# Optimization experiments

Measured on AMD Instinct MI355X. Metric: run time of the kernel, lower is better.

## Reference

```python
import jax, jax.numpy as jnp
import numpy as np
import math

B, T, E, K, V = 64, 512, 512, 512, 512


def setup_inputs() -> dict:
    key = jax.random.key(0)
    ks = jax.random.split(key, 7)
    s = 1.0 / math.sqrt(E)
    return {
        "x": jax.random.normal(ks[0], (B, T, E), dtype=jnp.float32),
        "Wq": jax.random.normal(ks[1], (E, K), dtype=jnp.float32) * s,
        "bq": jnp.zeros((K,), dtype=jnp.float32),
        "Wk": jax.random.normal(ks[2], (E, K), dtype=jnp.float32) * s,
        "bk": jnp.zeros((K,), dtype=jnp.float32),
        "Wv": jax.random.normal(ks[3], (E, V), dtype=jnp.float32) * s,
        "bv": jnp.zeros((V,), dtype=jnp.float32),
    }


def reference(x, Wq, bq, Wk, bk, Wv, bv):
    # Linear projections (N, T, E) -> (N, T, K/V)
    q = x @ Wq + bq
    k = x @ Wk + bk
    v = x @ Wv + bv
    # weight_pos_graph(query, keys) interpreted as Q K^T: (N, T, T)
    scores = jnp.einsum("btd,bsd->bts", q, k)
    # mask[j, i] = 1 if i > j  -> strict upper triangle masked to -inf (causal)
    mask = jnp.triu(jnp.ones((T, T), dtype=bool), k=1)
    scores = jnp.where(mask, -jnp.inf, scores)
    # NOTE: original softmaxes over dim=1 (the query/row axis), not dim=-1
    attn = jax.nn.softmax(scores / math.sqrt(K), axis=1)
    # bmm(attn, values): (N, T, T) @ (N, T, V) -> (N, T, V)
    return jnp.einsum("bts,bsv->btv", attn, v)
```

## Files before the change

### kernel.cpp

```cpp
#include <hip/hip_runtime.h>
#include <hip/hip_bf16.h>
#include <math.h>

#define B_DIM 64
#define T_DIM 512
#define E_DIM 512

typedef __bf16 bf16_t;
typedef bf16_t bf16x8 __attribute__((ext_vector_type(8)));
typedef float  f32x4  __attribute__((ext_vector_type(4)));

typedef unsigned char __attribute__((address_space(1))) uc_g;
typedef unsigned char __attribute__((address_space(3))) uc_l;

__device__ __forceinline__ void gl_lds16(const void* g, void* l) {
  __builtin_amdgcn_global_load_lds((const uc_g*)g, (uc_l*)l, 16, 0, 0);
}

__global__ __launch_bounds__(256) void cvtx_kernel(const float* __restrict__ x,
                                                   bf16_t* __restrict__ xb) {
  const size_t t = (size_t)blockIdx.x * 256 + threadIdx.x;
  const float4 a = ((const float4*)x)[t * 2];
  const float4 b = ((const float4*)x)[t * 2 + 1];
  bf16x8 o;
  o[0] = (bf16_t)a.x; o[1] = (bf16_t)a.y; o[2] = (bf16_t)a.z; o[3] = (bf16_t)a.w;
  o[4] = (bf16_t)b.x; o[5] = (bf16_t)b.y; o[6] = (bf16_t)b.z; o[7] = (bf16_t)b.w;
  *(bf16x8*)(xb + t * 8) = o;
}

__global__ __launch_bounds__(256) void wtr_kernel(const float* __restrict__ W0,
                                                  const float* __restrict__ W1,
                                                  const float* __restrict__ W2,
                                                  bf16_t* __restrict__ WTall) {
  const int z = blockIdx.z;
  const float* W = z == 0 ? W0 : (z == 1 ? W1 : W2);
  bf16_t* O = WTall + (size_t)z * 512 * E_DIM;
  __shared__ float tile[32][33];
  const int tx = threadIdx.x, ty = threadIdx.y;
  const int r0 = blockIdx.y * 32, c0 = blockIdx.x * 32;
#pragma unroll
  for (int i = 0; i < 4; ++i)
    tile[ty + i * 8][tx] = W[(size_t)(r0 + ty + i * 8) * E_DIM + c0 + tx];
  __syncthreads();
#pragma unroll
  for (int i = 0; i < 4; ++i)
    O[(size_t)(c0 + ty + i * 8) * E_DIM + r0 + tx] = (bf16_t)tile[tx][ty + i * 8];
}

__global__ __launch_bounds__(256) void bcat_kernel(const float* __restrict__ b0,
                                                   const float* __restrict__ b1,
                                                   const float* __restrict__ b2,
                                                   float* __restrict__ bb) {
  const int i = blockIdx.x * 256 + threadIdx.x;
  bb[i] = i < 512 ? b0[i] : (i < 1024 ? b1[i - 512] : b2[i - 1024]);
}

__global__ __launch_bounds__(256) void zero_kernel(float4* __restrict__ p) {
  p[blockIdx.x * 256 + threadIdx.x] = make_float4(0.f, 0.f, 0.f, 0.f);
}

__global__ __launch_bounds__(512) void vtr_kernel(const bf16_t* __restrict__ Vb,
                                                  const float* __restrict__ Dsum,
                                                  bf16_t* __restrict__ VT, int ldv) {
  const int b = blockIdx.z;
  __shared__ bf16_t tile[64][65];
  const int tx = threadIdx.x, ty = threadIdx.y;
  const bf16_t* src = Vb + (size_t)b * T_DIM * ldv;
  const float* Ds = Dsum + (size_t)b * T_DIM;
  bf16_t* dst = VT + (size_t)b * T_DIM * T_DIM;
  const int r0 = blockIdx.y * 64, c0 = blockIdx.x * 64;
#pragma unroll
  for (int i = 0; i < 8; ++i) {
    const int s = r0 + ty + i * 8;
    const float inv = 1.0f / Ds[s];
    tile[ty + i * 8][tx] = (bf16_t)((float)src[(size_t)s * ldv + c0 + tx] * inv);
  }
  __syncthreads();
#pragma unroll
  for (int i = 0; i < 8; ++i)
    dst[(size_t)(c0 + ty + i * 8) * T_DIM + r0 + tx] = tile[tx][ty + i * 8];
}

template <int EPI>
__global__ __launch_bounds__(512)
void gemm_p(const bf16_t* __restrict__ A, const bf16_t* __restrict__ Bt,
            void* __restrict__ Cv, const float* __restrict__ bias,
            float* __restrict__ Dsum,
            int lda, int ldb, int ldc, long sA, long sB, long sC, float scale) {
  __shared__ bf16_t lds[3][12288];
  const int tid = threadIdx.x;

  int bm, bn, bz, NT;
  if (EPI == 0) {
    const int lin = blockIdx.x;
    const int nl = (lin & 7) * 192 + (lin >> 3);
    bm = nl / 6; bn = nl - bm * 6;
    bz = 0; NT = 16;
  } else {
    bm = blockIdx.x; bn = blockIdx.y; bz = blockIdx.z;
    if (EPI == 1 && 2 * bn > bm) return;
    NT = (EPI == 2) ? (bm + 1) * 4 : 16;
  }

  const bf16_t* Ab = A + bz * sA + (long)bm * 128 * lda;
  const bf16_t* Bb = Bt + bz * sB + (long)bn * 256 * ldb;

  const int strow = tid >> 2, stg = tid & 3;
  const int sgg = stg ^ ((strow >> 1) & 3);
  const bf16_t* gA  = Ab + (long)strow * lda + sgg * 8;
  const bf16_t* gB0 = Bb + (long)strow * ldb + sgg * 8;
  const bf16_t* gB1 = gB0 + (long)128 * ldb;

#define STAGE(kt, buf) { gl_lds16(gA  + (long)(kt) * 32, &lds[buf][tid * 8]);        \
                         gl_lds16(gB0 + (long)(kt) * 32, &lds[buf][4096 + tid * 8]); \
                         gl_lds16(gB1 + (long)(kt) * 32, &lds[buf][8192 + tid * 8]); }

  const int l15 = tid & 15, lk = (tid >> 4) & 3;
  const int w = tid >> 6, wr = w >> 2, wc = w & 3;
  int aoff[4], boff[4];
#pragma unroll
  for (int m = 0; m < 4; ++m) {
    const int row = wr * 64 + m * 16 + l15;
    aoff[m] = row * 32 + (lk ^ ((row >> 1) & 3)) * 8;
  }
#pragma unroll
  for (int n = 0; n < 4; ++n) {
    const int row = wc * 64 + n * 16 + l15;
    boff[n] = 4096 + row * 32 + (lk ^ ((row >> 1) & 3)) * 8;
  }

  f32x4 acc[4][4] = {};

  STAGE(0, 0); STAGE(1, 1);
  asm volatile("s_waitcnt vmcnt(3)" ::: "memory");
  asm volatile("s_barrier" ::: "memory");

  int cb = 0;
  for (int kt = 0; kt < NT; ++kt) {
    bf16x8 af[4], bfr[4];
#pragma unroll
    for (int m = 0; m < 4; ++m) af[m] = *(const bf16x8*)&lds[cb][aoff[m]];
#pragma unroll
    for (int n = 0; n < 4; ++n) bfr[n] = *(const bf16x8*)&lds[cb][boff[n]];
    const int sb = (cb == 0) ? 2 : cb - 1;
    if (kt + 2 < NT) {
      STAGE(kt + 2, sb);
      asm volatile("s_waitcnt vmcnt(3)" ::: "memory");
    } else if (kt + 2 == NT) {
      asm volatile("s_waitcnt vmcnt(0)" ::: "memory");
    }
    asm volatile("s_barrier" ::: "memory");
    __builtin_amdgcn_s_setprio(1);
#pragma unroll
    for (int m = 0; m < 4; ++m)
#pragma unroll
      for (int n = 0; n < 4; ++n)
        acc[m][n] = __builtin_amdgcn_mfma_f32_16x16x32_bf16(af[m], bfr[n], acc[m][n], 0, 0, 0);
    __builtin_amdgcn_s_setprio(0);
    asm volatile("s_barrier" ::: "memory");
    cb = (cb == 2) ? 0 : cb + 1;
  }
#undef STAGE

  if constexpr (EPI == 0) {
    bf16_t* C = (bf16_t*)Cv;
#pragma unroll
    for (int m = 0; m < 4; ++m) {
      const long row0 = (long)bm * 128 + wr * 64 + m * 16 + lk * 4;
#pragma unroll
      for (int n = 0; n < 4; ++n) {
        const int col = bn * 256 + wc * 64 + n * 16 + l15;
        const float bv = bias[col];
#pragma unroll
        for (int r = 0; r < 4; ++r)
          C[(row0 + r) * (long)ldc + col] = (bf16_t)(acc[m][n][r] + bv);
      }
    }
  } else if constexpr (EPI == 1) {
    bf16_t* C = (bf16_t*)Cv + bz * sC;
    float ts[4] = {0.f, 0.f, 0.f, 0.f};
#pragma unroll
    for (int m = 0; m < 4; ++m) {
      const long row0 = (long)bm * 128 + wr * 64 + m * 16 + lk * 4;
#pragma unroll
      for (int n = 0; n < 4; ++n) {
        const int lcol = wc * 64 + n * 16 + l15;
        const int col = bn * 256 + lcol;
#pragma unroll
        for (int r = 0; r < 4; ++r) {
          const long row = row0 + r;
          float e = 0.f;
          if (col <= row) e = __expf(acc[m][n][r] * scale);
          const bf16_t eb = (bf16_t)e;
          C[row * (long)ldc + col] = eb;
          ts[n] += (float)eb;
        }
      }
    }
#pragma unroll
    for (int n = 0; n < 4; ++n) {
      ts[n] += __shfl_xor(ts[n], 16);
      ts[n] += __shfl_xor(ts[n], 32);
    }
    float* colsum = (float*)&lds[0][0];
    if (tid < 256) colsum[tid] = 0.f;
    __syncthreads();
    if (lk == 0) {
#pragma unroll
      for (int n = 0; n < 4; ++n)
        atomicAdd(&colsum[wc * 64 + n * 16 + l15], ts[n]);
    }
    __syncthreads();
    if (tid < 256)
      atomicAdd(&Dsum[(long)bz * T_DIM + bn * 256 + tid], colsum[tid]);
  } else {
    float* C = (float*)Cv + bz * sC;
#pragma unroll
    for (int m = 0; m < 4; ++m) {
      const long row0 = (long)bm * 128 + wr * 64 + m * 16 + lk * 4;
#pragma unroll
      for (int n = 0; n < 4; ++n) {
        const int col = bn * 256 + wc * 64 + n * 16 + l15;
#pragma unroll
        for (int r = 0; r < 4; ++r)
          C[(row0 + r) * (long)ldc + col] = acc[m][n][r];
      }
    }
  }
}

extern "C" void kernel_launch(void* const* d_in, const int* in_sizes, int n_in,
                              void* d_out, int out_size, void* d_ws, size_t ws_size,
                              hipStream_t stream) {
  const float* x  = (const float*)d_in[0];
  const float* Wq = (const float*)d_in[1];
  const float* bq = (const float*)d_in[2];
  const float* Wk = (const float*)d_in[3];
  const float* bk = (const float*)d_in[4];
  const float* Wv = (const float*)d_in[5];
  const float* bv = (const float*)d_in[6];
  float* out = (float*)d_out;

  char* ws = (char*)d_ws;
  const size_t SZ = (size_t)B_DIM * T_DIM * E_DIM * 2;
  bf16_t* xb    = (bf16_t*)(ws);
  bf16_t* P     = (bf16_t*)(ws);
  bf16_t* qkv   = (bf16_t*)(ws + SZ);
  bf16_t* vT    = (bf16_t*)(ws + SZ + 3 * SZ);
  bf16_t* WTall = (bf16_t*)(ws + 5 * SZ);
  float*  bcat  = (float*)(ws + 5 * SZ + 1572864);
  float*  Dsum  = (float*)(ws + 5 * SZ + 1572864 + 8192);

  const long sQKV = (long)T_DIM * 1536;
  const long bstr = (long)T_DIM * T_DIM;
  const float scale = 1.0f / sqrtf((float)E_DIM);

  cvtx_kernel<<<dim3(8192), dim3(256), 0, stream>>>(x, xb);
  wtr_kernel<<<dim3(16, 16, 3), dim3(32, 8), 0, stream>>>(Wq, Wk, Wv, WTall);
  bcat_kernel<<<dim3(6), dim3(256), 0, stream>>>(bq, bk, bv, bcat);
  gemm_p<0><<<dim3(1536), dim3(512), 0, stream>>>(
      xb, WTall, qkv, bcat, nullptr, 512, 512, 1536, 0, 0, 0, 0.f);
  zero_kernel<<<dim3(32), dim3(256), 0, stream>>>((float4*)Dsum);
  gemm_p<1><<<dim3(4, 2, B_DIM), dim3(512), 0, stream>>>(
      qkv, qkv + 512, P, nullptr, Dsum, 1536, 1536, T_DIM, sQKV, sQKV, bstr, scale);
  vtr_kernel<<<dim3(8, 8, B_DIM), dim3(64, 8), 0, stream>>>(qkv + 1024, Dsum, vT, 1536);
  gemm_p<2><<<dim3(4, 2, B_DIM), dim3(512), 0, stream>>>(
      P, vT, out, nullptr, nullptr, 512, 512, T_DIM, bstr, bstr, bstr, 1.f);
}
```

Before: 276.0 us.

## Merge prep kernels into one launch and use 256x256 tiled QKV GEMM

Four small preprocessing kernels (x conversion, weight transpose, bias concat, Dsum zeroing) are fused into one prep kernel dispatched by block index, removing launch overhead. The QKV projection moves from the generic 128x256 tile GEMM to a dedicated 256x256 tile kernel with a 64-wide K step, double-buffered 128KB LDS and interleaved half-tile loads and MFMA phases. This raises per-block data reuse and halves the block count, at the cost of one block per CU and more barriers per step.

```diff
diff --git a/kernel.cpp b/kernel.cpp
--- a/kernel.cpp
+++ b/kernel.cpp
@@ -17,46 +17,48 @@
   __builtin_amdgcn_global_load_lds((const uc_g*)g, (uc_l*)l, 16, 0, 0);
 }
 
-__global__ __launch_bounds__(256) void cvtx_kernel(const float* __restrict__ x,
-                                                   bf16_t* __restrict__ xb) {
-  const size_t t = (size_t)blockIdx.x * 256 + threadIdx.x;
-  const float4 a = ((const float4*)x)[t * 2];
-  const float4 b = ((const float4*)x)[t * 2 + 1];
-  bf16x8 o;
-  o[0] = (bf16_t)a.x; o[1] = (bf16_t)a.y; o[2] = (bf16_t)a.z; o[3] = (bf16_t)a.w;
-  o[4] = (bf16_t)b.x; o[5] = (bf16_t)b.y; o[6] = (bf16_t)b.z; o[7] = (bf16_t)b.w;
-  *(bf16x8*)(xb + t * 8) = o;
-}
-
-__global__ __launch_bounds__(256) void wtr_kernel(const float* __restrict__ W0,
-                                                  const float* __restrict__ W1,
-                                                  const float* __restrict__ W2,
-                                                  bf16_t* __restrict__ WTall) {
-  const int z = blockIdx.z;
-  const float* W = z == 0 ? W0 : (z == 1 ? W1 : W2);
-  bf16_t* O = WTall + (size_t)z * 512 * E_DIM;
+__global__ __launch_bounds__(256)
+void prep_kernel(const float* __restrict__ x,
+                 const float* __restrict__ Wq, const float* __restrict__ Wk,
+                 const float* __restrict__ Wv,
+                 const float* __restrict__ bq, const float* __restrict__ bk,
+                 const float* __restrict__ bv,
+                 bf16_t* __restrict__ xb, bf16_t* __restrict__ WTall,
+                 float* __restrict__ bcat, float* __restrict__ Dsum) {
   __shared__ float tile[32][33];
-  const int tx = threadIdx.x, ty = threadIdx.y;
-  const int r0 = blockIdx.y * 32, c0 = blockIdx.x * 32;
-#pragma unroll
-  for (int i = 0; i < 4; ++i)
-    tile[ty + i * 8][tx] = W[(size_t)(r0 + ty + i * 8) * E_DIM + c0 + tx];
-  __syncthreads();
-#pragma unroll
-  for (int i = 0; i < 4; ++i)
-    O[(size_t)(c0 + ty + i * 8) * E_DIM + r0 + tx] = (bf16_t)tile[tx][ty + i * 8];
-}
-
-__global__ __launch_bounds__(256) void bcat_kernel(const float* __restrict__ b0,
-                                                   const float* __restrict__ b1,
-                                                   const float* __restrict__ b2,
-                                                   float* __restrict__ bb) {
-  const int i = blockIdx.x * 256 + threadIdx.x;
-  bb[i] = i < 512 ? b0[i] : (i < 1024 ? b1[i - 512] : b2[i - 1024]);
-}
-
-__global__ __launch_bounds__(256) void zero_kernel(float4* __restrict__ p) {
-  p[blockIdx.x * 256 + threadIdx.x] = make_float4(0.f, 0.f, 0.f, 0.f);
+  const int bx = blockIdx.x;
+  const int t = threadIdx.x;
+  if (bx < 8192) {
+    const size_t i = (size_t)bx * 256 + t;
+    const float4 a = ((const float4*)x)[i * 2];
+    const float4 b = ((const float4*)x)[i * 2 + 1];
+    bf16x8 o;
+    o[0] = (bf16_t)a.x; o[1] = (bf16_t)a.y; o[2] = (bf16_t)a.z; o[3] = (bf16_t)a.w;
+    o[4] = (bf16_t)b.x; o[5] = (bf16_t)b.y; o[6] = (bf16_t)b.z; o[7] = (bf16_t)b.w;
+    *(bf16x8*)(xb + i * 8) = o;
+  } else if (bx < 8960) {
+    const int bid = bx - 8192;
+    const int z = bid >> 8;
+    const int tl = bid & 255;
+    const int c0 = (tl & 15) * 32, r0 = (tl >> 4) * 32;
+    const float* W = z == 0 ? Wq : (z == 1 ? Wk : Wv);
+    bf16_t* O = WTall + (size_t)z * 512 * E_DIM;
+    const int tx = t & 31, ty = t >> 5;
+#pragma unroll
+    for (int i = 0; i < 4; ++i)
+      tile[ty + i * 8][tx] = W[(size_t)(r0 + ty + i * 8) * E_DIM + c0 + tx];
+    __syncthreads();
+#pragma unroll
+    for (int i = 0; i < 4; ++i)
+      O[(size_t)(c0 + ty + i * 8) * E_DIM + r0 + tx] = (bf16_t)tile[tx][ty + i * 8];
+  } else if (bx == 8960) {
+#pragma unroll
+    for (int i = t; i < 1536; i += 256)
+      bcat[i] = i < 512 ? bq[i] : (i < 1024 ? bk[i - 512] : bv[i - 1024]);
+  } else {
+    const int i = (bx - 8961) * 256 + t;
+    ((float4*)Dsum)[i] = make_float4(0.f, 0.f, 0.f, 0.f);
+  }
 }
 
 __global__ __launch_bounds__(512) void vtr_kernel(const bf16_t* __restrict__ Vb,
@@ -81,6 +83,120 @@
     dst[(size_t)(c0 + ty + i * 8) * T_DIM + r0 + tx] = tile[tx][ty + i * 8];
 }
 
+__global__ __launch_bounds__(512)
+void gemm8p_qkv(const bf16_t* __restrict__ A, const bf16_t* __restrict__ Bt,
+                bf16_t* __restrict__ C, const float* __restrict__ bias) {
+  __shared__ bf16_t lds[65536];
+  const int tid = threadIdx.x;
+
+  const int lin = blockIdx.x;
+  const int nl = (lin & 7) * 96 + (lin >> 3);
+  const int bm = nl / 6, bn = nl - bm * 6;
+
+  const int sg = (tid & 3) ^ ((tid >> 3) & 3);
+  const bf16_t* gA = A + ((long)bm * 256 + (tid >> 2)) * 512 + sg * 8;
+  const bf16_t* gB = Bt + ((long)bn * 256 + (tid >> 2)) * 512 + sg * 8;
+
+#define STG(T, regoff, gp, kh) {                                          \
+    bf16_t* d_ = &lds[(((T) & 1) << 15) + (regoff) + tid * 8];            \
+    gl_lds16((gp) + (long)(T) * 64 + (kh) * 32, d_);                      \
+    gl_lds16((gp) + (long)(T) * 64 + (kh) * 32 + (long)128 * 512, d_ + 4096); }
+#define STG_Ak0(T) STG(T, 0,     gA, 0)
+#define STG_Ak1(T) STG(T, 8192,  gA, 1)
+#define STG_Bk0(T) STG(T, 16384, gB, 0)
+#define STG_Bk1(T) STG(T, 24576, gB, 1)
+
+  const int l15 = tid & 15, lk = (tid >> 4) & 3;
+  const int w = tid >> 6, wr = w >> 2, wc = w & 3;
+  int aoffs[8], boffs[4];
+#pragma unroll
+  for (int mm = 0; mm < 8; ++mm) {
+    const int row = wr * 128 + mm * 16 + l15;
+    aoffs[mm] = row * 32 + (lk ^ ((row >> 1) & 3)) * 8;
+  }
+#pragma unroll
+  for (int n = 0; n < 4; ++n) {
+    const int row = wc * 64 + n * 16 + l15;
+    boffs[n] = row * 32 + (lk ^ ((row >> 1) & 3)) * 8;
+  }
+
+  f32x4 acc[8][4] = {};
+
+  STG_Bk0(0); STG_Ak0(0); STG_Bk1(0); STG_Ak1(0);
+  STG_Bk0(1); STG_Ak0(1); STG_Bk1(1);
+  asm volatile("s_waitcnt vmcnt(6)" ::: "memory");
+  asm volatile("s_barrier" ::: "memory");
+
+#define MFMA16(BASE, AF, BF)                                                    \
+  __builtin_amdgcn_s_setprio(1);                                                \
+  _Pragma("unroll") for (int m_ = 0; m_ < 4; ++m_)                              \
+    _Pragma("unroll") for (int n_ = 0; n_ < 4; ++n_)                            \
+      acc[(BASE) + m_][n_] =                                                    \
+        __builtin_amdgcn_mfma_f32_16x16x32_bf16(AF[m_], BF[n_], acc[(BASE) + m_][n_], 0, 0, 0); \
+  __builtin_amdgcn_s_setprio(0);
+
+  for (int kt = 0; kt < 8; ++kt) {
+    const int bb = (kt & 1) << 15;
+    bf16x8 a[4], b0[4], b1[4];
+
+#pragma unroll
+    for (int n = 0; n < 4; ++n) b0[n] = *(const bf16x8*)&lds[bb + 16384 + boffs[n]];
+#pragma unroll
+    for (int m = 0; m < 4; ++m) a[m] = *(const bf16x8*)&lds[bb + aoffs[m]];
+    if (kt + 1 < 8) STG_Ak1(kt + 1);
+    asm volatile("s_barrier" ::: "memory");
+    MFMA16(0, a, b0);
+    asm volatile("s_barrier" ::: "memory");
+
+#pragma unroll
+    for (int m = 0; m < 4; ++m) a[m] = *(const bf16x8*)&lds[bb + aoffs[4 + m]];
+    if (kt + 2 < 8) STG_Bk0(kt + 2);
+    asm volatile("s_barrier" ::: "memory");
+    MFMA16(4, a, b0);
+    asm volatile("s_barrier" ::: "memory");
+
+#pragma unroll
+    for (int n = 0; n < 4; ++n) b1[n] = *(const bf16x8*)&lds[bb + 24576 + boffs[n]];
+#pragma unroll
+    for (int m = 0; m < 4; ++m) a[m] = *(const bf16x8*)&lds[bb + 8192 + aoffs[m]];
+    if (kt + 2 < 8) STG_Ak0(kt + 2);
+    asm volatile("s_barrier" ::: "memory");
+    MFMA16(0, a, b1);
+    asm volatile("s_barrier" ::: "memory");
+
+#pragma unroll
+    for (int m = 0; m < 4; ++m) a[m] = *(const bf16x8*)&lds[bb + 8192 + aoffs[4 + m]];
+    if (kt + 2 < 8) {
+      STG_Bk1(kt + 2);
+      asm volatile("s_waitcnt vmcnt(6)" ::: "memory");
+    } else if (kt + 1 < 8) {
+      asm volatile("s_waitcnt vmcnt(0)" ::: "memory");
+    }
+    asm volatile("s_barrier" ::: "memory");
+    MFMA16(4, a, b1);
+    asm volatile("s_barrier" ::: "memory");
+  }
+#undef MFMA16
+#undef STG_Ak0
+#undef STG_Ak1
+#undef STG_Bk0
+#undef STG_Bk1
+#undef STG
+
+#pragma unroll
+  for (int mm = 0; mm < 8; ++mm) {
+    const long row0 = (long)bm * 256 + wr * 128 + mm * 16 + lk * 4;
+#pragma unroll
+    for (int n = 0; n < 4; ++n) {
+      const int col = bn * 256 + wc * 64 + n * 16 + l15;
+      const float bv = bias[col];
+#pragma unroll
+      for (int r = 0; r < 4; ++r)
+        C[(row0 + r) * 1536 + col] = (bf16_t)(acc[mm][n][r] + bv);
+    }
+  }
+}
+
 template <int EPI>
 __global__ __launch_bounds__(512)
 void gemm_p(const bf16_t* __restrict__ A, const bf16_t* __restrict__ Bt,
@@ -91,16 +207,9 @@
   const int tid = threadIdx.x;
 
   int bm, bn, bz, NT;
-  if (EPI == 0) {
-    const int lin = blockIdx.x;
-    const int nl = (lin & 7) * 192 + (lin >> 3);
-    bm = nl / 6; bn = nl - bm * 6;
-    bz = 0; NT = 16;
-  } else {
-    bm = blockIdx.x; bn = blockIdx.y; bz = blockIdx.z;
-    if (EPI == 1 && 2 * bn > bm) return;
-    NT = (EPI == 2) ? (bm + 1) * 4 : 16;
-  }
+  bm = blockIdx.x; bn = blockIdx.y; bz = blockIdx.z;
+  if (EPI == 1 && 2 * bn > bm) return;
+  NT = (EPI == 2) ? (bm + 1) * 4 : 16;
 
   const bf16_t* Ab = A + bz * sA + (long)bm * 128 * lda;
   const bf16_t* Bb = Bt + bz * sB + (long)bn * 256 * ldb;
@@ -162,30 +271,15 @@
   }
 #undef STAGE
 
-  if constexpr (EPI == 0) {
-    bf16_t* C = (bf16_t*)Cv;
+  if constexpr (EPI == 1) {
+    bf16_t* C = (bf16_t*)Cv + bz * sC;
+    float ts[4] = {0.f, 0.f, 0.f, 0.f};
 #pragma unroll
     for (int m = 0; m < 4; ++m) {
       const long row0 = (long)bm * 128 + wr * 64 + m * 16 + lk * 4;
 #pragma unroll
       for (int n = 0; n < 4; ++n) {
         const int col = bn * 256 + wc * 64 + n * 16 + l15;
-        const float bv = bias[col];
-#pragma unroll
-        for (int r = 0; r < 4; ++r)
-          C[(row0 + r) * (long)ldc + col] = (bf16_t)(acc[m][n][r] + bv);
-      }
-    }
-  } else if constexpr (EPI == 1) {
-    bf16_t* C = (bf16_t*)Cv + bz * sC;
-    float ts[4] = {0.f, 0.f, 0.f, 0.f};
-#pragma unroll
-    for (int m = 0; m < 4; ++m) {
-      const long row0 = (long)bm * 128 + wr * 64 + m * 16 + lk * 4;
-#pragma unroll
-      for (int n = 0; n < 4; ++n) {
-        const int lcol = wc * 64 + n * 16 + l15;
-        const int col = bn * 256 + lcol;
 #pragma unroll
         for (int r = 0; r < 4; ++r) {
           const long row = row0 + r;
@@ -255,12 +349,9 @@
   const long bstr = (long)T_DIM * T_DIM;
   const float scale = 1.0f / sqrtf((float)E_DIM);
 
-  cvtx_kernel<<<dim3(8192), dim3(256), 0, stream>>>(x, xb);
-  wtr_kernel<<<dim3(16, 16, 3), dim3(32, 8), 0, stream>>>(Wq, Wk, Wv, WTall);
-  bcat_kernel<<<dim3(6), dim3(256), 0, stream>>>(bq, bk, bv, bcat);
-  gemm_p<0><<<dim3(1536), dim3(512), 0, stream>>>(
-      xb, WTall, qkv, bcat, nullptr, 512, 512, 1536, 0, 0, 0, 0.f);
-  zero_kernel<<<dim3(32), dim3(256), 0, stream>>>((float4*)Dsum);
+  prep_kernel<<<dim3(8993), dim3(256), 0, stream>>>(
+      x, Wq, Wk, Wv, bq, bk, bv, xb, WTall, bcat, Dsum);
+  gemm8p_qkv<<<dim3(768), dim3(512), 0, stream>>>(xb, WTall, qkv, bcat);
   gemm_p<1><<<dim3(4, 2, B_DIM), dim3(512), 0, stream>>>(
       qkv, qkv + 512, P, nullptr, Dsum, 1536, 1536, T_DIM, sQKV, sQKV, bstr, scale);
   vtr_kernel<<<dim3(8, 8, B_DIM), dim3(64, 8), 0, stream>>>(qkv + 1024, Dsum, vT, 1536);
```

Result: no change. 273.5 us (-0.9%).
